# Kernel tuning notes

Measured on AMD Instinct MI355X. Metric: run time of the kernel, lower is better.

The kernel has to match this reference:

```python
import jax, jax.numpy as jnp
import numpy as np

K = 16          # neighbors used for attention (knn uses K+1 incl. self)
LRELU = 0.01    # torch LeakyReLU default negative_slope


def setup_inputs() -> dict:
    key = jax.random.key(0)
    ks = jax.random.split(key, 12)
    B, N = 4, 8192
    w = lambda k, shape: (jax.random.normal(k, shape, jnp.float32) * 0.05)
    inp = {
        "x": jax.random.normal(ks[0], (B, N, 3), jnp.float32),
        "global_feat": jax.random.normal(ks[1], (B, 1024), jnp.float32),  # unused by forward (matches source)
        # convs1 = MLP_CONV(3, [64,128]): Conv1d(3,64)+ReLU, Conv1d(64,128)
        "W1": w(ks[2], (64, 3)),    "b1": jnp.zeros((64,), jnp.float32),
        "W2": w(ks[3], (128, 64)),  "b2": jnp.zeros((128,), jnp.float32),
        # convs2: Conv2d(9,64,1x1)+LReLU, Conv2d(64,64,1x1)+LReLU, Conv2d(64,128,1x1)
        "Wc1": w(ks[4], (64, 9)),   "bc1": jnp.zeros((64,), jnp.float32),
        "Wc2": w(ks[5], (64, 64)),  "bc2": jnp.zeros((64,), jnp.float32),
        "Wc3": w(ks[6], (128, 64)), "bc3": jnp.zeros((128,), jnp.float32),
        # conv_query / conv_key: Conv2d(256,256,1x1)
        "Wq": w(ks[7], (256, 256)), "bq": jnp.zeros((256,), jnp.float32),
        "Wk": w(ks[8], (256, 256)), "bk": jnp.zeros((256,), jnp.float32),
    }
    return inp


def _lrelu(t):
    return jnp.where(t >= 0, t, LRELU * t)


def _forward(x, W1, b1, W2, b2, Wc1, bc1, Wc2, bc2, Wc3, bc3, Wq, bq, Wk, bk):
    # convs1: pointwise MLP on coords -> per-point features f [B,N,128]
    f = jax.nn.relu(jnp.einsum('bnc,oc->bno', x, W1) + b1)
    f = jnp.einsum('bnc,oc->bno', f, W2) + b2

    # knn_points(x, x, K=17): squared-distance matrix, nearest-first (self at slot 0)
    sq = jnp.sum(x * x, axis=-1)                              # [B,N]
    d2 = sq[:, :, None] + sq[:, None, :] - 2.0 * jnp.einsum('bnc,bmc->bnm', x, x)
    _, idx = jax.lax.top_k(-d2, K + 1)                        # [B,N,K+1]

    gather = jax.vmap(lambda a, i: a[i])                      # per-batch fancy gather
    knn_x = gather(x, idx)                                    # [B,N,K+1,3]
    knn_f = gather(f, idx)                                    # [B,N,K+1,128]

    rep = jnp.broadcast_to(x[:, :, None, :], knn_x.shape)     # repeat_x
    r = jnp.concatenate([rep, knn_x, rep - knn_x], axis=-1)   # [B,N,K+1,9]
    r = _lrelu(jnp.einsum('bnkc,oc->bnko', r, Wc1) + bc1)
    r = _lrelu(jnp.einsum('bnkc,oc->bnko', r, Wc2) + bc2)
    r = jnp.einsum('bnkc,oc->bnko', r, Wc3) + bc3             # [B,N,K+1,128]

    feat = jnp.concatenate([knn_f, r], axis=-1)               # [B,N,K+1,256]
    q = jnp.einsum('bnkc,oc->bnko', feat[:, :, :1, :], Wq) + bq   # [B,N,1,256]
    k = jnp.einsum('bnkc,oc->bnko', feat[:, :, 1:, :], Wk) + bk   # [B,N,K,256]
    w = jax.nn.softmax(jnp.sum(q * k, axis=-1), axis=-1)      # [B,N,K]
    new_x = jnp.sum(w[..., None] * knn_x[:, :, 1:, :], axis=2)    # [B,N,3]
    return new_x


def reference(x, global_feat, W1, b1, W2, b2, Wc1, bc1, Wc2, bc2, Wc3, bc3, Wq, bq, Wk, bk):
    del global_feat  # present in the torch signature but unused in forward
    return _forward(x, W1, b1, W2, b2, Wc1, bc1, Wc2, bc2, Wc3, bc3, Wq, bq, Wk, bk)
```

## Files before the change

kernel.cpp:

```cpp
#include <hip/hip_runtime.h>
#include <hip/hip_bf16.h>

#define NPTS 8192
#define NB   4

typedef unsigned short u16;
typedef unsigned int   u32;
typedef short bf16x8 __attribute__((ext_vector_type(8)));
typedef float f32x4  __attribute__((ext_vector_type(4)));

static __device__ __forceinline__ float bflo(u32 u){ return __uint_as_float(u << 16); }
static __device__ __forceinline__ float bfhi(u32 u){ return __uint_as_float(u & 0xffff0000u); }
static __device__ __forceinline__ u16 f2bf(float f){
  u32 x = __float_as_uint(f);
  return (u16)((x + 0x7fffu + ((x >> 16) & 1u)) >> 16);
}
static __device__ __forceinline__ float lrelu(float v){ return v >= 0.f ? v : 0.01f * v; }

__global__ __launch_bounds__(256) void k0_prep(const float* __restrict__ Wq, const float* __restrict__ bq,
                                               const float* __restrict__ Wk, const float* __restrict__ Wc3,
                                               const float* __restrict__ Wc2,
                                               u16* __restrict__ Mb, float* __restrict__ u,
                                               u16* __restrict__ Wc3T, u16* __restrict__ Wc2p){
  int oc = blockIdx.x, c = threadIdx.x;
  float acc = 0.f;
  for (int r = 0; r < 256; ++r) acc = fmaf(Wk[r*256 + oc], Wq[r*256 + c], acc);
  Mb[oc*256 + c] = f2bf(acc);
  __shared__ float red[256];
  red[c] = Wk[c*256 + oc] * bq[c];
  __syncthreads();
  for (int s = 128; s > 0; s >>= 1){ if (c < s) red[c] += red[c + s]; __syncthreads(); }
  if (c == 0) u[oc] = red[0];
  if (oc < 32){ int e = oc*256 + c; int h = e >> 7, o = e & 127; Wc3T[h*128 + o] = f2bf(Wc3[o*64 + h]); }
  if (oc >= 32 && oc < 48){ int e = (oc - 32)*256 + c; Wc2p[e] = f2bf(Wc2[e]); }
}

__global__ __launch_bounds__(128) void k1_feat(const float* __restrict__ x, const float* __restrict__ W1,
                                               const float* __restrict__ b1, const float* __restrict__ W2,
                                               const float* __restrict__ b2, u16* __restrict__ f){
  __shared__ float xs[16][4];
  __shared__ float hids[16][68];
  __shared__ float W2s[128][68];
  int b = blockIdx.y; int n0 = blockIdx.x * 16; int t = threadIdx.x;
  const float* xb = x + ((size_t)b*NPTS + n0)*3;
  if (t < 48){ int p = t/3, c = t - p*3; xs[p][c] = xb[p*3 + c]; }
  for (int e = t; e < 8192; e += 128) W2s[e >> 6][e & 63] = W2[e];
  __syncthreads();
  {
    int e = t;
    #pragma unroll
    for (int ii = 0; ii < 8; ++ii, e += 128){
      int p = e >> 6, h = e & 63;
      float v = b1[h];
      v = fmaf(W1[h*3+0], xs[p][0], v);
      v = fmaf(W1[h*3+1], xs[p][1], v);
      v = fmaf(W1[h*3+2], xs[p][2], v);
      hids[p][h] = v > 0.f ? v : 0.f;
    }
  }
  __syncthreads();
  int p = t >> 3, og = t & 7;
  float acc[16];
  #pragma unroll
  for (int i = 0; i < 16; ++i) acc[i] = b2[og + 8*i];
  #pragma unroll 4
  for (int c4 = 0; c4 < 16; ++c4){
    float4 hv = *(const float4*)&hids[p][c4*4];
    #pragma unroll
    for (int i = 0; i < 16; ++i){
      float4 wv = *(const float4*)&W2s[og + 8*i][c4*4];
      acc[i] = fmaf(wv.x, hv.x, acc[i]); acc[i] = fmaf(wv.y, hv.y, acc[i]);
      acc[i] = fmaf(wv.z, hv.z, acc[i]); acc[i] = fmaf(wv.w, hv.w, acc[i]);
    }
  }
  u16* fb = f + ((size_t)b*NPTS + n0)*128;
  #pragma unroll
  for (int i = 0; i < 16; ++i) fb[p*128 + og + 8*i] = f2bf(acc[i]);
}

#define K2_FLUSH8() do { \
    _Pragma("unroll") \
    for (int s = 0; s < 8; ++s){ \
      int2 pr = *(const int2*)(bufp + s*4096); \
      float d = (s < cnt) ? __int_as_float(pr.x) : __builtin_inff(); \
      int ii = pr.y; \
      bool pk = bd[16] > d; \
      _Pragma("unroll") \
      for (int k = 16; k >= 1; --k){ \
        bool pk1 = bd[k-1] > d; \
        float nd = pk1 ? bd[k-1] : d; \
        int   ni = pk1 ? bi[k-1] : ii; \
        if (pk){ bd[k] = nd; bi[k] = ni; } \
        pk = pk1; \
      } \
      if (pk){ bd[0] = d; bi[0] = ii; } \
    } \
    cnt = 0; } while (0)

__global__ __launch_bounds__(512) void k2_knn(const float* __restrict__ x, int* __restrict__ idxout){
#pragma clang fp contract(off)
  __shared__ __align__(16) char smem[69632];
  int t = threadIdx.x, lane = t & 63, w = t >> 6;
  int b = blockIdx.y;
  const float* xb = x + (size_t)b*NPTS*3;
  int q = blockIdx.x*64 + lane;
  float qx = xb[q*3+0], qy = xb[q*3+1], qz = xb[q*3+2];
  float qsq = (qx*qx + qy*qy) + qz*qz;
  float bd[17]; int bi[17];
  #pragma unroll
  for (int k = 0; k < 17; ++k){ bd[k] = __builtin_inff(); bi[k] = 0; }
  float4* tile = (float4*)smem;
  float*  tauv = (float*)(smem + 8192);
  char*   bufp = smem + 10240 + t*8;
  tauv[t] = __builtin_inff();
  __syncthreads();
  int cnt = 0;
  float gate = __builtin_inff();
  int c0 = w * 1024;
  for (int t0 = 0; t0 < 1024; t0 += 64){
    int m = c0 + t0 + lane;
    float cx = xb[m*3+0], cy = xb[m*3+1], cz = xb[m*3+2];
    float csq = (cx*cx + cy*cy) + cz*cz;
    tile[w*64 + lane] = make_float4(cx, cy, cz, csq);
    for (int j0 = 0; j0 < 64; j0 += 4){
      float d2v[4];
      #pragma unroll
      for (int s = 0; s < 4; ++s){
        float4 cd = tile[w*64 + j0 + s];
        float dt = (qx*cd.x + qy*cd.y) + qz*cd.z;
        d2v[s] = (qsq + cd.w) - 2.0f*dt;
      }
      float mn = fminf(fminf(d2v[0], d2v[1]), fminf(d2v[2], d2v[3]));
      if (__any(mn < gate)){
        #pragma unroll
        for (int s = 0; s < 4; ++s){
          if (d2v[s] < gate){
            *(int2*)(bufp + cnt*4096) = make_int2(__float_as_int(d2v[s]), c0 + t0 + j0 + s);
            ++cnt;
          }
        }
        if (__any(cnt >= 5)){
          K2_FLUSH8();
          gate = fminf(gate, bd[16]);
          tauv[t] = bd[16];
        }
      }
    }
    tauv[t] = bd[16];
    float tm = fminf(tauv[lane], tauv[64 + lane]);
    tm = fminf(tm, fminf(tauv[128 + lane], tauv[192 + lane]));
    tm = fminf(tm, fminf(tauv[256 + lane], tauv[320 + lane]));
    tm = fminf(tm, fminf(tauv[384 + lane], tauv[448 + lane]));
    gate = fminf(tm, bd[16]);
  }
  K2_FLUSH8();
  __syncthreads();
  float* md = (float*)smem;
  int*   mi = (int*)(smem + 34816);
  {
    int base = (w*64 + lane)*17;
    #pragma unroll
    for (int k = 0; k < 17; ++k){ md[base + k] = bd[k]; mi[base + k] = bi[k]; }
  }
  __syncthreads();
  if (w == 0){
    int p0=0,p1=0,p2=0,p3=0,p4=0,p5=0,p6=0,p7=0;
    int* op = idxout + ((size_t)b*NPTS + q)*17;
    int base = lane*17;
    for (int k = 0; k < 17; ++k){
      float h0 = md[        base + p0];
      float h1 = md[1088  + base + p1];
      float h2 = md[2176  + base + p2];
      float h3 = md[3264  + base + p3];
      float h4 = md[4352  + base + p4];
      float h5 = md[5440  + base + p5];
      float h6 = md[6528  + base + p6];
      float h7 = md[7616  + base + p7];
      float best = h0; int ws = 0;
      if (h1 < best){ best = h1; ws = 1; }
      if (h2 < best){ best = h2; ws = 2; }
      if (h3 < best){ best = h3; ws = 3; }
      if (h4 < best){ best = h4; ws = 4; }
      if (h5 < best){ best = h5; ws = 5; }
      if (h6 < best){ best = h6; ws = 6; }
      if (h7 < best){ best = h7; ws = 7; }
      int pp = (ws==0)?p0:(ws==1)?p1:(ws==2)?p2:(ws==3)?p3:(ws==4)?p4:(ws==5)?p5:(ws==6)?p6:p7;
      op[k] = mi[ws*1088 + base + pp];
      p0 += (ws==0); p1 += (ws==1); p2 += (ws==2); p3 += (ws==3);
      p4 += (ws==4); p5 += (ws==5); p6 += (ws==6); p7 += (ws==7);
    }
  }
}

__global__ __launch_bounds__(256) void k3_qt(const float* __restrict__ x, const int* __restrict__ idx,
    const u16* __restrict__ f, const u16* __restrict__ Mb, const float* __restrict__ u,
    const u16* __restrict__ Wc3T,
    const float* __restrict__ Wc1, const float* __restrict__ bc1,
    const float* __restrict__ Wc2, const float* __restrict__ bc2,
    const float* __restrict__ bc3, float* __restrict__ qg){
  __shared__ __align__(16) char smem[73088];
  u16*   featb = (u16*)smem;
  float* qtBs  = (float*)(smem + 16896);
  float* h1s   = (float*)(smem + 16896);
  float* h2s   = (float*)(smem + 25600);
  float* Wc1s  = (float*)(smem + 34304);
  float* Wc2s  = (float*)(smem + 36608);
  u16*   W3sD  = (u16*)(smem + 36608);
  u16*   W3s   = (u16*)(smem + 54016);
  float* bcs   = (float*)(smem + 71424);
  float* xns   = (float*)(smem + 71936);
  float* xgs   = (float*)(smem + 72448);
  int*   idx0s = (int*)(smem + 72960);

  int b = blockIdx.y; int n0 = blockIdx.x * 32; int t = threadIdx.x;
  const int p3 = t >> 3, hg = t & 7;

  if (t < 32) idx0s[t] = idx[((size_t)b*NPTS + n0 + t)*17];
  {
    const float* xb = x + ((size_t)b*NPTS + n0)*3;
    if (t < 96){ int p = t/3, c = t - p*3; xns[p*4 + c] = xb[p*3 + c]; }
  }
  if (t < 128) bcs[t] = (t < 64) ? bc1[t] : bc2[t - 64];
  for (int e = t; e < 576; e += 256) Wc1s[e] = Wc1[e];
  for (int e = t; e < 4096; e += 256) Wc2s[(e >> 6)*68 + (e & 63)] = Wc2[e];
  __syncthreads();
  if (t < 96){ int p = t/3, c = t - p*3; xgs[p*4 + c] = x[((size_t)b*NPTS + idx0s[p])*3 + c]; }
  {
    int cg = t & 7;
    const uint4* fsrc = (const uint4*)(f + ((size_t)b*NPTS + idx0s[p3])*128) + cg*2;
    uint4 A = fsrc[0], B = fsrc[1];
    uint4* dst = (uint4*)&featb[p3*264 + cg*16];
    dst[0] = A; dst[1] = B;
  }
  __syncthreads();
  {
    float rv0 = xns[p3*4+0], rv1 = xns[p3*4+1], rv2 = xns[p3*4+2];
    float rv3 = xgs[p3*4+0], rv4 = xgs[p3*4+1], rv5 = xgs[p3*4+2];
    float rv6 = rv0 - rv3, rv7 = rv1 - rv4, rv8 = rv2 - rv5;
    #pragma unroll
    for (int i = 0; i < 8; ++i){
      int h = hg + 8*i;
      const float* wr = &Wc1s[h*9];
      float v = bcs[h];
      v = fmaf(wr[0], rv0, v); v = fmaf(wr[1], rv1, v); v = fmaf(wr[2], rv2, v);
      v = fmaf(wr[3], rv3, v); v = fmaf(wr[4], rv4, v); v = fmaf(wr[5], rv5, v);
      v = fmaf(wr[6], rv6, v); v = fmaf(wr[7], rv7, v); v = fmaf(wr[8], rv8, v);
      h1s[p3*68 + h] = lrelu(v);
    }
  }
  __syncthreads();
  {
    #pragma unroll
    for (int i = 0; i < 8; ++i){
      int h = hg + 8*i;
      float v = bcs[64 + h];
      const float* wr = &Wc2s[h*68];
      const float* ar = &h1s[p3*68];
      #pragma unroll
      for (int c4 = 0; c4 < 16; ++c4){
        float4 wv = *(const float4*)(wr + c4*4);
        float4 av = *(const float4*)(ar + c4*4);
        v = fmaf(wv.x, av.x, v); v = fmaf(wv.y, av.y, v);
        v = fmaf(wv.z, av.z, v); v = fmaf(wv.w, av.w, v);
      }
      h2s[p3*68 + h] = lrelu(v);
    }
  }
  __syncthreads();
  for (int e = t; e < 4096; e += 256) *(u32*)&W3s[(e >> 6)*136 + (e & 63)*2] = ((const u32*)Wc3T)[e];
  __syncthreads();
  {
    int og = hg;
    float4 a0 = *(const float4*)&bc3[og*16 + 0];
    float4 a1 = *(const float4*)&bc3[og*16 + 4];
    float4 a2 = *(const float4*)&bc3[og*16 + 8];
    float4 a3 = *(const float4*)&bc3[og*16 + 12];
    for (int h = 0; h < 64; ++h){
      float hv = h2s[p3*68 + h];
      const u32* wp = (const u32*)&W3s[h*136 + og*16];
      uint4 A = *(const uint4*)wp; uint4 B = *(const uint4*)(wp + 4);
      a0.x = fmaf(bflo(A.x), hv, a0.x); a0.y = fmaf(bfhi(A.x), hv, a0.y);
      a0.z = fmaf(bflo(A.y), hv, a0.z); a0.w = fmaf(bfhi(A.y), hv, a0.w);
      a1.x = fmaf(bflo(A.z), hv, a1.x); a1.y = fmaf(bfhi(A.z), hv, a1.y);
      a1.z = fmaf(bflo(A.w), hv, a1.z); a1.w = fmaf(bfhi(A.w), hv, a1.w);
      a2.x = fmaf(bflo(B.x), hv, a2.x); a2.y = fmaf(bfhi(B.x), hv, a2.y);
      a2.z = fmaf(bflo(B.y), hv, a2.z); a2.w = fmaf(bfhi(B.y), hv, a2.w);
      a3.x = fmaf(bflo(B.z), hv, a3.x); a3.y = fmaf(bfhi(B.z), hv, a3.y);
      a3.z = fmaf(bflo(B.w), hv, a3.z); a3.w = fmaf(bfhi(B.w), hv, a3.w);
    }
    u16* dst = &featb[p3*264 + 128 + og*16];
    u32 pw[8];
    pw[0] = (u32)f2bf(a0.x) | ((u32)f2bf(a0.y) << 16);
    pw[1] = (u32)f2bf(a0.z) | ((u32)f2bf(a0.w) << 16);
    pw[2] = (u32)f2bf(a1.x) | ((u32)f2bf(a1.y) << 16);
    pw[3] = (u32)f2bf(a1.z) | ((u32)f2bf(a1.w) << 16);
    pw[4] = (u32)f2bf(a2.x) | ((u32)f2bf(a2.y) << 16);
    pw[5] = (u32)f2bf(a2.z) | ((u32)f2bf(a2.w) << 16);
    pw[6] = (u32)f2bf(a3.x) | ((u32)f2bf(a3.y) << 16);
    pw[7] = (u32)f2bf(a3.z) | ((u32)f2bf(a3.w) << 16);
    ((uint4*)dst)[0] = make_uint4(pw[0], pw[1], pw[2], pw[3]);
    ((uint4*)dst)[1] = make_uint4(pw[4], pw[5], pw[6], pw[7]);
  }
  __syncthreads();
  {
    int lane = t & 63, wv = t >> 6;
    int l15 = lane & 15, kq = lane >> 4;
    f32x4 acc[2][4];
    #pragma unroll
    for (int rt = 0; rt < 2; ++rt)
      #pragma unroll
      for (int ct = 0; ct < 4; ++ct)
        acc[rt][ct] = (f32x4){0.f, 0.f, 0.f, 0.f};
    #pragma unroll
    for (int ks = 0; ks < 8; ++ks){
      bf16x8 a0 = *(const bf16x8*)&featb[l15*264 + ks*32 + kq*8];
      bf16x8 a1 = *(const bf16x8*)&featb[(16 + l15)*264 + ks*32 + kq*8];
      #pragma unroll
      for (int ct = 0; ct < 4; ++ct){
        int oc = wv*64 + ct*16 + l15;
        bf16x8 bb = *(const bf16x8*)(Mb + oc*256 + ks*32 + kq*8);
        acc[0][ct] = __builtin_amdgcn_mfma_f32_16x16x32_bf16(a0, bb, acc[0][ct], 0, 0, 0);
        acc[1][ct] = __builtin_amdgcn_mfma_f32_16x16x32_bf16(a1, bb, acc[1][ct], 0, 0, 0);
      }
    }
    if (wv < 2){
      float* qgb = qg + ((size_t)b*NPTS + n0)*192;
      #pragma unroll
      for (int ct = 0; ct < 4; ++ct){
        int oc = wv*64 + ct*16 + l15;
        float uv = u[oc];
        #pragma unroll
        for (int rt = 0; rt < 2; ++rt){
          #pragma unroll
          for (int j = 0; j < 4; ++j){
            int p = rt*16 + kq*4 + j;
            qgb[(size_t)p*192 + oc] = acc[rt][ct][j] + uv;
          }
        }
      }
    } else {
      #pragma unroll
      for (int ct = 0; ct < 4; ++ct){
        int oc = (wv - 2)*64 + ct*16 + l15;
        float uv = u[128 + oc];
        #pragma unroll
        for (int rt = 0; rt < 2; ++rt){
          #pragma unroll
          for (int j = 0; j < 4; ++j){
            int p = rt*16 + kq*4 + j;
            qtBs[p*132 + oc] = acc[rt][ct][j] + uv;
          }
        }
      }
    }
  }
  __syncthreads();
  for (int e = t; e < 4096; e += 256) *(u32*)&W3sD[(e >> 6)*136 + (e & 63)*2] = ((const u32*)Wc3T)[e];
  __syncthreads();
  {
    float gacc[8];
    #pragma unroll
    for (int i = 0; i < 8; ++i) gacc[i] = 0.f;
    for (int o8 = 0; o8 < 16; ++o8){
      const float* qr = &qtBs[p3*132 + o8*8];
      float4 qa = *(const float4*)qr; float4 qb4 = *(const float4*)(qr + 4);
      #pragma unroll
      for (int i = 0; i < 8; ++i){
        int h = hg + 8*i;
        const uint4 WU = *(const uint4*)&W3sD[h*136 + o8*8];
        float acc = gacc[i];
        acc = fmaf(bflo(WU.x), qa.x, acc); acc = fmaf(bfhi(WU.x), qa.y, acc);
        acc = fmaf(bflo(WU.y), qa.z, acc); acc = fmaf(bfhi(WU.y), qa.w, acc);
        acc = fmaf(bflo(WU.z), qb4.x, acc); acc = fmaf(bfhi(WU.z), qb4.y, acc);
        acc = fmaf(bflo(WU.w), qb4.z, acc); acc = fmaf(bfhi(WU.w), qb4.w, acc);
        gacc[i] = acc;
      }
    }
    float* qgb = qg + ((size_t)b*NPTS + n0)*192;
    #pragma unroll
    for (int i = 0; i < 8; ++i) qgb[p3*192 + 128 + hg + 8*i] = gacc[i];
  }
}

__global__ __launch_bounds__(256) void k4_attn(const float* __restrict__ x, const int* __restrict__ idx,
    const u16* __restrict__ f, const float* __restrict__ qg,
    const float* __restrict__ Wc1, const float* __restrict__ bc1,
    const float* __restrict__ bc2, const u16* __restrict__ Wc2p,
    float* __restrict__ out){
  __shared__ int   idxs[16][17];
  __shared__ float xns[16][4];
  __shared__ float qgs[16][196];
  __shared__ float Wc1s[576];
  __shared__ float bcs[128];
  __shared__ float xjs[256][4];
  __shared__ float flog[256];
  __shared__ u16   h1t[256][76];
  int b = blockIdx.y; int n0 = blockIdx.x * 16; int t = threadIdx.x;
  for (int e = t; e < 272; e += 256){ int p = e/17, k = e - p*17; idxs[p][k] = idx[((size_t)b*NPTS + n0 + p)*17 + k]; }
  if (t < 48){ int p = t/3, c = t - p*3; xns[p][c] = x[((size_t)b*NPTS + n0 + p)*3 + c]; }
  if (t < 128) bcs[t] = (t < 64) ? bc1[t] : bc2[t - 64];
  for (int e = t; e < 576; e += 256) Wc1s[e] = Wc1[e];
  {
    const float* src = qg + ((size_t)b*NPTS + n0)*192;
    for (int e = t; e < 3072; e += 256){ int p = e/192, c = e - p*192; qgs[p][c] = src[e]; }
  }
  __syncthreads();
  {
    int p = t >> 4, j = t & 15;
    int nidx = idxs[p][j + 1];
    const float* xr = x + ((size_t)b*NPTS + nidx)*3;
    float cx = xr[0], cy = xr[1], cz = xr[2];
    *(float4*)&xjs[t][0] = make_float4(cx, cy, cz, 0.f);
    float rx = xns[p][0], ry = xns[p][1], rz = xns[p][2];
    float dx = rx - cx, dy = ry - cy, dz = rz - cz;
    float logit = 0.f;
    {
      const u32* fr = (const u32*)(f + ((size_t)b*NPTS + nidx)*128);
      #pragma unroll
      for (int c8 = 0; c8 < 16; ++c8){
        uint4 FU = *(const uint4*)(fr + c8*4);
        const float* qr = &qgs[p][c8*8];
        float4 qa = *(const float4*)qr; float4 qb4 = *(const float4*)(qr + 4);
        logit = fmaf(bflo(FU.x), qa.x, logit); logit = fmaf(bfhi(FU.x), qa.y, logit);
        logit = fmaf(bflo(FU.y), qa.z, logit); logit = fmaf(bfhi(FU.y), qa.w, logit);
        logit = fmaf(bflo(FU.z), qb4.x, logit); logit = fmaf(bfhi(FU.z), qb4.y, logit);
        logit = fmaf(bflo(FU.w), qb4.z, logit); logit = fmaf(bfhi(FU.w), qb4.w, logit);
      }
    }
    flog[t] = logit;
    float h1r[64];
    #pragma unroll
    for (int h = 0; h < 64; ++h){
      const float* wr = &Wc1s[h*9];
      float v = bcs[h];
      v = fmaf(wr[0], rx, v); v = fmaf(wr[1], ry, v); v = fmaf(wr[2], rz, v);
      v = fmaf(wr[3], cx, v); v = fmaf(wr[4], cy, v); v = fmaf(wr[5], cz, v);
      v = fmaf(wr[6], dx, v); v = fmaf(wr[7], dy, v); v = fmaf(wr[8], dz, v);
      h1r[h] = lrelu(v);
    }
    u16* hrow = &h1t[t][0];
    #pragma unroll
    for (int c8 = 0; c8 < 8; ++c8){
      u32 w0 = (u32)f2bf(h1r[c8*8+0]) | ((u32)f2bf(h1r[c8*8+1]) << 16);
      u32 w1 = (u32)f2bf(h1r[c8*8+2]) | ((u32)f2bf(h1r[c8*8+3]) << 16);
      u32 w2 = (u32)f2bf(h1r[c8*8+4]) | ((u32)f2bf(h1r[c8*8+5]) << 16);
      u32 w3 = (u32)f2bf(h1r[c8*8+6]) | ((u32)f2bf(h1r[c8*8+7]) << 16);
      *(uint4*)&hrow[c8*8] = make_uint4(w0, w1, w2, w3);
    }
  }
  __syncthreads();
  {
    int lane = t & 63, wv = t >> 6;
    int l15 = lane & 15, kq = lane >> 4;
    f32x4 acc[4][4];
    #pragma unroll
    for (int rt = 0; rt < 4; ++rt)
      #pragma unroll
      for (int ct = 0; ct < 4; ++ct)
        acc[rt][ct] = (f32x4){0.f, 0.f, 0.f, 0.f};
    #pragma unroll
    for (int ks = 0; ks < 2; ++ks){
      bf16x8 av[4];
      #pragma unroll
      for (int rt = 0; rt < 4; ++rt)
        av[rt] = *(const bf16x8*)&h1t[wv*64 + rt*16 + l15][ks*32 + kq*8];
      #pragma unroll
      for (int ct = 0; ct < 4; ++ct){
        bf16x8 bv = *(const bf16x8*)(Wc2p + (ct*16 + l15)*64 + ks*32 + kq*8);
        #pragma unroll
        for (int rt = 0; rt < 4; ++rt)
          acc[rt][ct] = __builtin_amdgcn_mfma_f32_16x16x32_bf16(av[rt], bv, acc[rt][ct], 0, 0, 0);
      }
    }
    float lg[4][4];
    #pragma unroll
    for (int rt = 0; rt < 4; ++rt)
      #pragma unroll
      for (int reg = 0; reg < 4; ++reg) lg[rt][reg] = 0.f;
    #pragma unroll
    for (int ct = 0; ct < 4; ++ct){
      int col = ct*16 + l15;
      float b2v = bcs[64 + col];
      #pragma unroll
      for (int rt = 0; rt < 4; ++rt){
        float gv = qgs[wv*4 + rt][128 + col];
        #pragma unroll
        for (int reg = 0; reg < 4; ++reg){
          float h2 = lrelu(acc[rt][ct][reg] + b2v);
          lg[rt][reg] = fmaf(gv, h2, lg[rt][reg]);
        }
      }
    }
    #pragma unroll
    for (int s = 1; s < 16; s <<= 1){
      #pragma unroll
      for (int rt = 0; rt < 4; ++rt)
        #pragma unroll
        for (int reg = 0; reg < 4; ++reg)
          lg[rt][reg] += __shfl_xor(lg[rt][reg], s, 64);
    }
    #pragma unroll
    for (int rt = 0; rt < 4; ++rt){
      float4 fl = *(const float4*)&flog[(wv*4 + rt)*16 + kq*4];
      float l0 = lg[rt][0] + fl.x, l1 = lg[rt][1] + fl.y;
      float l2 = lg[rt][2] + fl.z, l3 = lg[rt][3] + fl.w;
      float mx = fmaxf(fmaxf(l0, l1), fmaxf(l2, l3));
      mx = fmaxf(mx, __shfl_xor(mx, 16, 64));
      mx = fmaxf(mx, __shfl_xor(mx, 32, 64));
      float e0 = expf(l0 - mx), e1 = expf(l1 - mx), e2 = expf(l2 - mx), e3 = expf(l3 - mx);
      float sm = (e0 + e1) + (e2 + e3);
      sm += __shfl_xor(sm, 16, 64);
      sm += __shfl_xor(sm, 32, 64);
      int rbase = (wv*4 + rt)*16 + kq*4;
      float4 x0 = *(const float4*)&xjs[rbase + 0][0];
      float4 x1 = *(const float4*)&xjs[rbase + 1][0];
      float4 x2 = *(const float4*)&xjs[rbase + 2][0];
      float4 x3 = *(const float4*)&xjs[rbase + 3][0];
      float ox = e0*x0.x + e1*x1.x + e2*x2.x + e3*x3.x;
      float oy = e0*x0.y + e1*x1.y + e2*x2.y + e3*x3.y;
      float oz = e0*x0.z + e1*x1.z + e2*x2.z + e3*x3.z;
      ox += __shfl_xor(ox, 16, 64); ox += __shfl_xor(ox, 32, 64);
      oy += __shfl_xor(oy, 16, 64); oy += __shfl_xor(oy, 32, 64);
      oz += __shfl_xor(oz, 16, 64); oz += __shfl_xor(oz, 32, 64);
      if (kq == 0 && l15 == rt){
        float inv = 1.f / sm;
        float* op = out + ((size_t)b*NPTS + n0 + wv*4 + rt)*3;
        op[0] = ox * inv; op[1] = oy * inv; op[2] = oz * inv;
      }
    }
  }
}

extern "C" void kernel_launch(void* const* d_in, const int* in_sizes, int n_in,
                              void* d_out, int out_size, void* d_ws, size_t ws_size,
                              hipStream_t stream){
  (void)in_sizes; (void)n_in; (void)out_size; (void)ws_size;
  const float* x   = (const float*)d_in[0];
  const float* W1  = (const float*)d_in[2];
  const float* b1  = (const float*)d_in[3];
  const float* W2  = (const float*)d_in[4];
  const float* b2  = (const float*)d_in[5];
  const float* Wc1 = (const float*)d_in[6];
  const float* bc1 = (const float*)d_in[7];
  const float* Wc2 = (const float*)d_in[8];
  const float* bc2 = (const float*)d_in[9];
  const float* Wc3 = (const float*)d_in[10];
  const float* bc3 = (const float*)d_in[11];
  const float* Wq  = (const float*)d_in[12];
  const float* bq  = (const float*)d_in[13];
  const float* Wk  = (const float*)d_in[14];
  float* out = (float*)d_out;

  char* ws = (char*)d_ws;
  u16*   Mb   = (u16*)(ws + 0);
  float* u    = (float*)(ws + 131072);
  u16*   Wc3T = (u16*)(ws + 132096);
  u16*   Wc2p = (u16*)(ws + 153600);
  u16*   fbuf = (u16*)(ws + (1u << 20));
  int*   idxb = (int*)(ws + (16u << 20));
  float* qgb  = (float*)(ws + (32u << 20));

  k0_prep<<<dim3(256), dim3(256), 0, stream>>>(Wq, bq, Wk, Wc3, Wc2, Mb, u, Wc3T, Wc2p);
  k1_feat<<<dim3(512, NB), dim3(128), 0, stream>>>(x, W1, b1, W2, b2, fbuf);
  k2_knn<<<dim3(128, NB), dim3(512), 0, stream>>>(x, idxb);
  k3_qt<<<dim3(256, NB), dim3(256), 0, stream>>>(x, idxb, fbuf, Mb, u, Wc3T, Wc1, bc1, Wc2, bc2, bc3, qgb);
  k4_attn<<<dim3(512, NB), dim3(256), 0, stream>>>(x, idxb, fbuf, qgb, Wc1, bc1, bc2, Wc2p, out);
}
```

Before: 457.1 us.

## Compute kNN distances with split-bf16 MFMA and exact fp32 rerank

The kNN kernel now computes query-candidate dot products with bf16 MFMA instructions, using a hi/lo split of the coordinates so the result approaches fp32 accuracy. A new pack kernel precomputes the candidate tiles. Each wave keeps 20 approximate candidates filtered by a gate with a small margin, then recomputes exact fp32 distances and reranks to the top 17 before the cross-wave merge. The block also shrinks from 8 to 4 waves, each scanning 2048 candidates. This targets the scalar distance-evaluation cost, at the risk of neighbor-ordering mismatches when the margin or the 20-candidate buffer is not enough.

Result: slower. 536.1 us (+17.3%).

```diff
diff --git a/kernel.cpp b/kernel.cpp
--- a/kernel.cpp
+++ b/kernel.cpp
@@ -78,116 +78,197 @@
   for (int i = 0; i < 16; ++i) fb[p*128 + og + 8*i] = f2bf(acc[i]);
 }
 
-#define K2_FLUSH8() do { \
-    _Pragma("unroll") \
-    for (int s = 0; s < 8; ++s){ \
-      int2 pr = *(const int2*)(bufp + s*4096); \
-      float d = (s < cnt) ? __int_as_float(pr.x) : __builtin_inff(); \
-      int ii = pr.y; \
-      bool pk = bd[16] > d; \
+__global__ __launch_bounds__(256) void k2p_pack(const float* __restrict__ x, u16* __restrict__ pk){
+  int gid = blockIdx.x*256 + threadIdx.x;
+  const float* xr = x + (size_t)gid*3;
+  float cx = xr[0], cy = xr[1], cz = xr[2];
+  float csq = (cx*cx + cy*cy) + cz*cz;
+  u16 h0 = f2bf(cx), h1 = f2bf(cy), h2 = f2bf(cz);
+  u16 l0 = f2bf(cx - bflo(h0)), l1 = f2bf(cy - bflo(h1)), l2 = f2bf(cz - bflo(h2));
+  u16 sh = f2bf(csq);
+  u16 sl = f2bf(csq - bflo(sh));
+  u32 w0 = (u32)h0 | ((u32)h1 << 16);
+  u32 w1 = (u32)h2 | ((u32)l0 << 16);
+  u32 w2 = (u32)l1 | ((u32)l2 << 16);
+  u32 w3 = (u32)h0 | ((u32)h1 << 16);
+  u32 w4 = (u32)h2 | ((u32)l0 << 16);
+  u32 w5 = (u32)l1 | ((u32)l2 << 16);
+  u32 w6 = (u32)sh | ((u32)sl << 16);
+  uint4* dst = (uint4*)(pk + (size_t)gid*32);
+  dst[0] = make_uint4(w0, w1, w2, w3);
+  dst[1] = make_uint4(w4, w5, w6, 0u);
+  dst[2] = make_uint4(0u, 0u, 0u, 0u);
+  dst[3] = make_uint4(0u, 0u, 0u, 0u);
+}
+
+#define K2_MARGIN 2e-3f
+
+#define K2_FLUSH20() do { \
+    _Pragma("clang loop unroll_count(1)") \
+    for (int s_ = 0; s_ < 8; ++s_){ \
+      int2 pr_ = *(const int2*)(pb + s_*2048); \
+      float d_ = (s_ < cnt) ? __int_as_float(pr_.x) : __builtin_inff(); \
+      int ii_ = pr_.y; \
+      bool pk_ = bd[19] > d_; \
       _Pragma("unroll") \
-      for (int k = 16; k >= 1; --k){ \
-        bool pk1 = bd[k-1] > d; \
-        float nd = pk1 ? bd[k-1] : d; \
-        int   ni = pk1 ? bi[k-1] : ii; \
-        if (pk){ bd[k] = nd; bi[k] = ni; } \
-        pk = pk1; \
+      for (int k_ = 19; k_ >= 1; --k_){ \
+        bool p1_ = bd[k_-1] > d_; \
+        float nd_ = p1_ ? bd[k_-1] : d_; \
+        int   ni_ = p1_ ? bi[k_-1] : ii_; \
+        if (pk_){ bd[k_] = nd_; bi[k_] = ni_; } \
+        pk_ = p1_; \
       } \
-      if (pk){ bd[0] = d; bi[0] = ii; } \
+      if (pk_){ bd[0] = d_; bi[0] = ii_; } \
     } \
     cnt = 0; } while (0)
 
-__global__ __launch_bounds__(512) void k2_knn(const float* __restrict__ x, int* __restrict__ idxout){
+#define K2_GATE() do { \
+    tauv[w*64 + lane] = bd[19]; \
+    float ta_ = tauv[lane], tb_ = tauv[64 + lane]; \
+    float tc_ = tauv[128 + lane], td_ = tauv[192 + lane]; \
+    gM = fminf(fminf(ta_, tb_), fminf(tc_, td_)) + K2_MARGIN; } while (0)
+
+__global__ __launch_bounds__(256, 3) void k2_knn(const float* __restrict__ x,
+                                                 const u16* __restrict__ pk,
+                                                 int* __restrict__ idxout){
 #pragma clang fp contract(off)
-  __shared__ __align__(16) char smem[69632];
+  __shared__ __align__(16) char smem[53248];
   int t = threadIdx.x, lane = t & 63, w = t >> 6;
-  int b = blockIdx.y;
+  int b = blockIdx.y, q0 = blockIdx.x*64;
   const float* xb = x + (size_t)b*NPTS*3;
-  int q = blockIdx.x*64 + lane;
-  float qx = xb[q*3+0], qy = xb[q*3+1], qz = xb[q*3+2];
+  const u16* pkb = pk + (size_t)b*NPTS*32;
+  u16*   qtab = (u16*)smem;
+  float* tauv = (float*)(smem + 4096);
+  float* Dtw  = (float*)(smem + 5120 + w*5376);
+  char*  pb   = smem + 26624 + t*8;
+  u16*   mi20 = (u16*)(smem + 43008);
+
+  if (t < 64){
+    const float* qq = xb + (q0 + t)*3;
+    float m0 = -2.f*qq[0], m1 = -2.f*qq[1], m2 = -2.f*qq[2];
+    u16 h0 = f2bf(m0), h1 = f2bf(m1), h2 = f2bf(m2);
+    u16 l0 = f2bf(m0 - bflo(h0)), l1 = f2bf(m1 - bflo(h1)), l2 = f2bf(m2 - bflo(h2));
+    u32 w0 = (u32)h0 | ((u32)h1 << 16);
+    u32 w1 = (u32)h2 | ((u32)h0 << 16);
+    u32 w2 = (u32)h1 | ((u32)h2 << 16);
+    u32 w3 = (u32)l0 | ((u32)l1 << 16);
+    u32 w4 = (u32)l2 | ((u32)l0 << 16);
+    u32 w5 = (u32)l1 | ((u32)l2 << 16);
+    u32 w6 = 0x3F803F80u;
+    uint4* qd = (uint4*)(qtab + t*32);
+    qd[0] = make_uint4(w0, w1, w2, w3);
+    qd[1] = make_uint4(w4, w5, w6, 0u);
+    qd[2] = make_uint4(0u, 0u, 0u, 0u);
+    qd[3] = make_uint4(0u, 0u, 0u, 0u);
+  }
+  tauv[t] = __builtin_inff();
+  int qown = q0 + lane;
+  float qx = xb[qown*3+0], qy = xb[qown*3+1], qz = xb[qown*3+2];
   float qsq = (qx*qx + qy*qy) + qz*qz;
-  float bd[17]; int bi[17];
+  __syncthreads();
+
+  int l15 = lane & 15, kq = lane >> 4;
+  bf16x8 afr[4];
   #pragma unroll
-  for (int k = 0; k < 17; ++k){ bd[k] = __builtin_inff(); bi[k] = 0; }
-  float4* tile = (float4*)smem;
-  float*  tauv = (float*)(smem + 8192);
-  char*   bufp = smem + 10240 + t*8;
-  tauv[t] = __builtin_inff();
-  __syncthreads();
+  for (int rt = 0; rt < 4; ++rt)
+    afr[rt] = *(const bf16x8*)&qtab[(rt*16 + l15)*32 + kq*8];
+
+  float bd[20]; int bi[20];
+  #pragma unroll
+  for (int k = 0; k < 20; ++k){ bd[k] = __builtin_inff(); bi[k] = 0; }
   int cnt = 0;
-  float gate = __builtin_inff();
-  int c0 = w * 1024;
-  for (int t0 = 0; t0 < 1024; t0 += 64){
-    int m = c0 + t0 + lane;
-    float cx = xb[m*3+0], cy = xb[m*3+1], cz = xb[m*3+2];
-    float csq = (cx*cx + cy*cy) + cz*cz;
-    tile[w*64 + lane] = make_float4(cx, cy, cz, csq);
-    for (int j0 = 0; j0 < 64; j0 += 4){
-      float d2v[4];
-      #pragma unroll
-      for (int s = 0; s < 4; ++s){
-        float4 cd = tile[w*64 + j0 + s];
-        float dt = (qx*cd.x + qy*cd.y) + qz*cd.z;
-        d2v[s] = (qsq + cd.w) - 2.0f*dt;
-      }
-      float mn = fminf(fminf(d2v[0], d2v[1]), fminf(d2v[2], d2v[3]));
-      if (__any(mn < gate)){
-        #pragma unroll
-        for (int s = 0; s < 4; ++s){
-          if (d2v[s] < gate){
-            *(int2*)(bufp + cnt*4096) = make_int2(__float_as_int(d2v[s]), c0 + t0 + j0 + s);
-            ++cnt;
-          }
+  float gM = __builtin_inff();
+  int c0 = w*2048;
+  const float* selbase = Dtw + kq*336 + l15;
+  const u16* pkt = pkb + (size_t)(c0 + l15)*32 + kq*8;
+  bf16x8 bb = *(const bf16x8*)pkt;
+
+  for (int t0 = 0; t0 < 128; ++t0){
+    bf16x8 bn = bb;
+    if (t0 < 127) bn = *(const bf16x8*)(pkt + 512);
+    pkt += 512;
+    f32x4 z = (f32x4){0.f, 0.f, 0.f, 0.f};
+    f32x4 dA = __builtin_amdgcn_mfma_f32_16x16x32_bf16(afr[0], bb, z, 0, 0, 0);
+    f32x4 dB = __builtin_amdgcn_mfma_f32_16x16x32_bf16(afr[1], bb, z, 0, 0, 0);
+    f32x4 dC = __builtin_amdgcn_mfma_f32_16x16x32_bf16(afr[2], bb, z, 0, 0, 0);
+    f32x4 dD = __builtin_amdgcn_mfma_f32_16x16x32_bf16(afr[3], bb, z, 0, 0, 0);
+    *(f32x4*)(Dtw + 0*336 + l15*20 + kq*4) = dA;
+    *(f32x4*)(Dtw + 1*336 + l15*20 + kq*4) = dB;
+    *(f32x4*)(Dtw + 2*336 + l15*20 + kq*4) = dC;
+    *(f32x4*)(Dtw + 3*336 + l15*20 + kq*4) = dD;
+    int cb = c0 + t0*16;
+    #pragma clang loop unroll_count(1)
+    for (int g = 0; g < 4; ++g){
+      #pragma unroll
+      for (int i = 0; i < 4; ++i){
+        float d2a = qsq + selbase[(g*4 + i)*20];
+        if (d2a < gM){
+          *(int2*)(pb + cnt*2048) = make_int2(__float_as_int(d2a), cb + g*4 + i);
+          ++cnt;
         }
-        if (__any(cnt >= 5)){
-          K2_FLUSH8();
-          gate = fminf(gate, bd[16]);
-          tauv[t] = bd[16];
-        }
-      }
-    }
-    tauv[t] = bd[16];
-    float tm = fminf(tauv[lane], tauv[64 + lane]);
-    tm = fminf(tm, fminf(tauv[128 + lane], tauv[192 + lane]));
-    tm = fminf(tm, fminf(tauv[256 + lane], tauv[320 + lane]));
-    tm = fminf(tm, fminf(tauv[384 + lane], tauv[448 + lane]));
-    gate = fminf(tm, bd[16]);
-  }
-  K2_FLUSH8();
-  __syncthreads();
-  float* md = (float*)smem;
-  int*   mi = (int*)(smem + 34816);
-  {
+      }
+      if (__any(cnt >= 5)){ K2_FLUSH20(); K2_GATE(); }
+    }
+    K2_GATE();
+    bb = bn;
+  }
+  K2_FLUSH20();
+  {
+    u16* myrow = mi20 + (w*64 + lane)*20;
+    #pragma unroll
+    for (int s = 0; s < 20; ++s)
+      myrow[s] = (bd[s] == __builtin_inff()) ? (u16)0xFFFF : (u16)bi[s];
+  }
+  __syncthreads();
+  float* md17 = (float*)smem;
+  int*   mi17 = (int*)(smem + 17408);
+  {
+    float nd2[17]; int ni2[17];
+    #pragma unroll
+    for (int k = 0; k < 17; ++k){ nd2[k] = __builtin_inff(); ni2[k] = 0; }
+    const u16* myrow = mi20 + (w*64 + lane)*20;
+    #pragma clang loop unroll_count(2)
+    for (int s = 0; s < 20; ++s){
+      u32 c16 = myrow[s];
+      int cc = (c16 == 0xFFFFu) ? 0 : (int)c16;
+      const float* cr = xb + cc*3;
+      float cx = cr[0], cy = cr[1], cz = cr[2];
+      float csq = (cx*cx + cy*cy) + cz*cz;
+      float dt = (qx*cx + qy*cy) + qz*cz;
+      float d2 = (qsq + csq) - 2.0f*dt;
+      d2 = (c16 == 0xFFFFu) ? __builtin_inff() : d2;
+      bool pk_ = nd2[16] > d2;
+      #pragma unroll
+      for (int k = 16; k >= 1; --k){
+        bool p1_ = nd2[k-1] > d2;
+        float nd_ = p1_ ? nd2[k-1] : d2;
+        int   ni_ = p1_ ? ni2[k-1] : cc;
+        if (pk_){ nd2[k] = nd_; ni2[k] = ni_; }
+        pk_ = p1_;
+      }
+      if (pk_){ nd2[0] = d2; ni2[0] = cc; }
+    }
     int base = (w*64 + lane)*17;
     #pragma unroll
-    for (int k = 0; k < 17; ++k){ md[base + k] = bd[k]; mi[base + k] = bi[k]; }
+    for (int k = 0; k < 17; ++k){ md17[base + k] = nd2[k]; mi17[base + k] = ni2[k]; }
   }
   __syncthreads();
   if (w == 0){
-    int p0=0,p1=0,p2=0,p3=0,p4=0,p5=0,p6=0,p7=0;
-    int* op = idxout + ((size_t)b*NPTS + q)*17;
+    int p0 = 0, p1 = 0, p2 = 0, p3 = 0;
+    int* op = idxout + ((size_t)b*NPTS + q0 + lane)*17;
     int base = lane*17;
     for (int k = 0; k < 17; ++k){
-      float h0 = md[        base + p0];
-      float h1 = md[1088  + base + p1];
-      float h2 = md[2176  + base + p2];
-      float h3 = md[3264  + base + p3];
-      float h4 = md[4352  + base + p4];
-      float h5 = md[5440  + base + p5];
-      float h6 = md[6528  + base + p6];
-      float h7 = md[7616  + base + p7];
+      float h0 = md17[       base + p0];
+      float h1 = md17[1088 + base + p1];
+      float h2 = md17[2176 + base + p2];
+      float h3 = md17[3264 + base + p3];
       float best = h0; int ws = 0;
       if (h1 < best){ best = h1; ws = 1; }
       if (h2 < best){ best = h2; ws = 2; }
       if (h3 < best){ best = h3; ws = 3; }
-      if (h4 < best){ best = h4; ws = 4; }
-      if (h5 < best){ best = h5; ws = 5; }
-      if (h6 < best){ best = h6; ws = 6; }
-      if (h7 < best){ best = h7; ws = 7; }
-      int pp = (ws==0)?p0:(ws==1)?p1:(ws==2)?p2:(ws==3)?p3:(ws==4)?p4:(ws==5)?p5:(ws==6)?p6:p7;
-      op[k] = mi[ws*1088 + base + pp];
+      int pp = (ws==0) ? p0 : (ws==1) ? p1 : (ws==2) ? p2 : p3;
+      op[k] = mi17[ws*1088 + base + pp];
       p0 += (ws==0); p1 += (ws==1); p2 += (ws==2); p3 += (ws==3);
-      p4 += (ws==4); p5 += (ws==5); p6 += (ws==6); p7 += (ws==7);
     }
   }
 }
@@ -558,11 +639,13 @@
   u16*   Wc2p = (u16*)(ws + 153600);
   u16*   fbuf = (u16*)(ws + (1u << 20));
   int*   idxb = (int*)(ws + (16u << 20));
+  u16*   pkb  = (u16*)(ws + (20u << 20));
   float* qgb  = (float*)(ws + (32u << 20));
 
   k0_prep<<<dim3(256), dim3(256), 0, stream>>>(Wq, bq, Wk, Wc3, Wc2, Mb, u, Wc3T, Wc2p);
   k1_feat<<<dim3(512, NB), dim3(128), 0, stream>>>(x, W1, b1, W2, b2, fbuf);
-  k2_knn<<<dim3(128, NB), dim3(512), 0, stream>>>(x, idxb);
+  k2p_pack<<<dim3(128), dim3(256), 0, stream>>>(x, pkb);
+  k2_knn<<<dim3(128, NB), dim3(256), 0, stream>>>(x, pkb, idxb);
   k3_qt<<<dim3(256, NB), dim3(256), 0, stream>>>(x, idxb, fbuf, Mb, u, Wc3T, Wc1, bc1, Wc2, bc2, bc3, qgb);
   k4_attn<<<dim3(512, NB), dim3(256), 0, stream>>>(x, idxb, fbuf, qgb, Wc1, bc1, bc2, Wc2p, out);
 }
```
